# Performance work log

Hardware: AMD Instinct MI355X
Metric: run time of the kernel (lower is better)

## Reference

```python
import jax, jax.numpy as jnp
import numpy as np

N_HEADS = 4
D_K = 64

def setup_inputs() -> dict:
    key = jax.random.key(0)
    k1, k2, k3 = jax.random.split(key, 3)
    B, C, H, W = 16, 256, 32, 32
    x = jax.random.normal(k1, (B, C, H, W), dtype=jnp.float32)
    # Linear(C, 3*n_heads*d_k) stored as [in, out] for x @ W
    w_proj = jax.random.normal(k2, (C, 3 * N_HEADS * D_K), dtype=jnp.float32) * (1.0 / np.sqrt(C))
    b_proj = jnp.zeros((3 * N_HEADS * D_K,), dtype=jnp.float32)
    w_out = jax.random.normal(k3, (N_HEADS * D_K, C), dtype=jnp.float32) * (1.0 / np.sqrt(N_HEADS * D_K))
    b_out = jnp.zeros((C,), dtype=jnp.float32)
    return {"x": x, "w_proj": w_proj, "b_proj": b_proj, "w_out": w_out, "b_out": b_out}

def reference(x, w_proj, b_proj, w_out, b_out):
    B, C, H, W = x.shape
    S = H * W
    scale = D_K ** -0.5
    xs = x.reshape(B, C, S).transpose(0, 2, 1)            # [B, S, C]
    qkv = (xs @ w_proj + b_proj).reshape(B, S, N_HEADS, 3 * D_K)
    q, k, v = jnp.split(qkv, 3, axis=3)                    # each [B, S, H, dk]
    attn = jnp.einsum('bihd,bjhd->bijh', q, k) * scale     # [B, S, S, heads]
    attn = jax.nn.softmax(attn, axis=2)
    o = jnp.einsum('bijh,bjhd->bihd', attn, v)             # [B, S, heads, dk]
    o = o.reshape(B, S, N_HEADS * D_K)
    res = o @ w_out + b_out + xs                           # [B, S, C]
    return res.transpose(0, 2, 1).reshape(B, C, H, W)
```

## Files before the change

kernel.cpp:

```cpp
#include <hip/hip_runtime.h>
#include <math.h>

#define B_  16
#define C_  256
#define S_  1024
#define NH  4
#define DK  64
#define P3  768
#define ND  256

typedef unsigned short u16;
typedef unsigned int   u32;
typedef float  f32x4  __attribute__((ext_vector_type(4)));
typedef short  bf16x8 __attribute__((ext_vector_type(8)));

#define MFMA16(a, b, c) __builtin_amdgcn_mfma_f32_16x16x32_bf16(a, b, c, 0, 0, 0)

#define QSCALE 0.1803368801111137f

#define WAITVM(N) asm volatile("s_waitcnt vmcnt(" #N ")" ::: "memory")
#define BARRIER() asm volatile("s_barrier" ::: "memory")

#if __has_builtin(__builtin_amdgcn_exp2f)
#define EXP2F(x) __builtin_amdgcn_exp2f(x)
#else
#define EXP2F(x) exp2f(x)
#endif

__device__ __forceinline__ u16 f2bf(float f) {
    union { float f; u32 u; } x; x.f = f;
    u32 r = x.u + 0x7fffu + ((x.u >> 16) & 1u);
    return (u16)(r >> 16);
}

__device__ __forceinline__ u32 cvtpk(float lo, float hi) {
    u32 r;
    asm("v_cvt_pk_bf16_f32 %0, %1, %2" : "=v"(r) : "v"(lo), "v"(hi));
    return r;
}

__device__ __forceinline__ void stage16(const u16* g, u16* l) {
    __builtin_amdgcn_global_load_lds(
        (const __attribute__((address_space(1))) void*)g,
        (__attribute__((address_space(3))) void*)l, 16, 0, 0);
}

__global__ __launch_bounds__(256) void transpose_w(
    const float* __restrict__ wp, u16* __restrict__ wpT,
    const float* __restrict__ wo, u16* __restrict__ woT)
{
    const int z = blockIdx.z;
    const int Cc = z ? 256 : 768;
    if ((int)blockIdx.x * 64 >= Cc) return;
    const float* src = z ? wo : wp;
    u16* dst = z ? woT : wpT;
    const int R = 256;

    __shared__ float T[64][65];
    const int tid = threadIdx.x;
    const int c0 = blockIdx.x * 64, r0 = blockIdx.y * 64;

    const int l64 = tid & 63, rr0 = tid >> 6;
    #pragma unroll
    for (int t = 0; t < 16; ++t) {
        int rr = rr0 + t * 4;
        T[rr][l64] = src[(size_t)(r0 + rr) * Cc + c0 + l64];
    }
    __syncthreads();
    const int rp = tid & 31;
    const int cb = tid >> 5;
    #pragma unroll
    for (int t = 0; t < 8; ++t) {
        int c = cb + t * 8;
        u32 lo = f2bf(T[2 * rp][c]);
        u32 hi = f2bf(T[2 * rp + 1][c]);
        *(u32*)&dst[(size_t)(c0 + c) * R + r0 + 2 * rp] = lo | (hi << 16);
    }
}

__global__ __launch_bounds__(256, 2) void qkv_fused(
    const float* __restrict__ x, const u16* __restrict__ wpT,
    const float* __restrict__ bp, u16* __restrict__ qo,
    u16* __restrict__ ko, u16* __restrict__ vo)
{
    __shared__ __align__(16) u16 SM[40960];

    const int tid = threadIdx.x;
    const int w = tid >> 6, lane = tid & 63;
    const int n_ = lane & 15, quad = lane >> 4;

    const int id  = blockIdx.x;
    const int nid = (id & 7) * 64 + (id >> 3);
    const int hd  = nid & 3;
    const int g   = nid >> 2;
    const int s0  = (g & 7) * 128;
    const int b   = g >> 3;
    const int bh  = b * NH + hd;

    const int kq8  = tid >> 5;
    const int row4 = tid & 31;
    const float* xb = x + ((size_t)b * C_ + kq8 * 8) * S_ + s0 + row4 * 4;

    int awaddr[4];
    {
        const int kc = kq8 >> 2, quadk = kq8 & 3;
        #pragma unroll
        for (int j = 0; j < 4; ++j) {
            int row = row4 * 4 + j;
            awaddr[j] = ((row >> 4) * 2 + kc) * 512 + quadk * 128 +
                        ((((row & 15) + (row >> 4)) & 15) * 8);
        }
    }

    const u16* brp[3];
    #pragma unroll
    for (int i = 0; i < 3; ++i)
        brp[i] = wpT + (size_t)(hd * 192 + (w * 3 + i) * 16 + n_) * C_ + quad * 8;

    f32x4 acc[2][12];
    #pragma unroll
    for (int am = 0; am < 2; ++am)
        #pragma unroll
        for (int nf = 0; nf < 12; ++nf)
            #pragma unroll
            for (int r = 0; r < 4; ++r) acc[am][nf][r] = 0.f;

    float4 av[8];

    #pragma unroll
    for (int ci = 0; ci < 8; ++ci)
        av[ci] = *(const float4*)(xb + (size_t)ci * S_);
    {
        u16* Bs0 = SM + 8192;
        #pragma unroll
        for (int i = 0; i < 3; ++i) {
            stage16(brp[i],      Bs0 + ((w * 3 + i) * 2 + 0) * 512);
            stage16(brp[i] + 32, Bs0 + ((w * 3 + i) * 2 + 1) * 512);
        }
    }
    #pragma unroll
    for (int j = 0; j < 4; ++j) {
        union { bf16x8 v; u32 u[4]; } pk;
        pk.u[0] = cvtpk(av[0][j], av[1][j]);
        pk.u[1] = cvtpk(av[2][j], av[3][j]);
        pk.u[2] = cvtpk(av[4][j], av[5][j]);
        pk.u[3] = cvtpk(av[6][j], av[7][j]);
        *(bf16x8*)&SM[awaddr[j]] = pk.v;
    }
    __syncthreads();

    #pragma unroll
    for (int p = 0; p < 4; ++p) {
        u16* As_ = SM + (p & 1) * 20480;
        u16* Bs_ = As_ + 8192;
        u16* An  = SM + ((p + 1) & 1) * 20480;
        u16* Bn  = An + 8192;

        if (p < 3) {
            #pragma unroll
            for (int ci = 0; ci < 8; ++ci)
                av[ci] = *(const float4*)(xb + ((size_t)(p + 1) * 64 + ci) * S_);
            #pragma unroll
            for (int i = 0; i < 3; ++i) {
                stage16(brp[i] + (p + 1) * 64,      Bn + ((w * 3 + i) * 2 + 0) * 512);
                stage16(brp[i] + (p + 1) * 64 + 32, Bn + ((w * 3 + i) * 2 + 1) * 512);
            }
        }

        #pragma unroll
        for (int kc = 0; kc < 2; ++kc) {
            bf16x8 af0 = *(const bf16x8*)&As_[((2 * w + 0) * 2 + kc) * 512 +
                                              quad * 128 + (((n_ + 2 * w + 0) & 15) * 8)];
            bf16x8 af1 = *(const bf16x8*)&As_[((2 * w + 1) * 2 + kc) * 512 +
                                              quad * 128 + (((n_ + 2 * w + 1) & 15) * 8)];
            #pragma unroll
            for (int nf = 0; nf < 12; ++nf) {
                bf16x8 bf = *(const bf16x8*)&Bs_[(nf * 2 + kc) * 512 + lane * 8];
                acc[0][nf] = MFMA16(af0, bf, acc[0][nf]);
                acc[1][nf] = MFMA16(af1, bf, acc[1][nf]);
            }
        }

        if (p < 3) {
            #pragma unroll
            for (int j = 0; j < 4; ++j) {
                union { bf16x8 v; u32 u[4]; } pk;
                pk.u[0] = cvtpk(av[0][j], av[1][j]);
                pk.u[1] = cvtpk(av[2][j], av[3][j]);
                pk.u[2] = cvtpk(av[4][j], av[5][j]);
                pk.u[3] = cvtpk(av[6][j], av[7][j]);
                *(bf16x8*)&An[awaddr[j]] = pk.v;
            }
        }
        __syncthreads();
    }

    float bias[12];
    #pragma unroll
    for (int nf = 0; nf < 12; ++nf) bias[nf] = bp[hd * 192 + nf * 16 + n_];

    u16* Cq = SM;
    u16* Ck = SM + 9216;
    u16* Cv = SM + 18432;

    #pragma unroll
    for (int am = 0; am < 2; ++am) {
        int row0 = w * 32 + am * 16 + quad * 4;
        #pragma unroll
        for (int nf = 0; nf < 4; ++nf)
            #pragma unroll
            for (int r = 0; r < 4; ++r)
                Cq[(row0 + r) * 72 + nf * 16 + n_] =
                    f2bf((acc[am][nf][r] + bias[nf]) * QSCALE);
        #pragma unroll
        for (int nf = 4; nf < 8; ++nf)
            #pragma unroll
            for (int r = 0; r < 4; ++r)
                Ck[(row0 + r) * 72 + (nf - 4) * 16 + n_] =
                    f2bf(acc[am][nf][r] + bias[nf]);
        int colb = w * 32 + am * 16 + quad * 4;
        #pragma unroll
        for (int nf = 8; nf < 12; ++nf)
            #pragma unroll
            for (int r = 0; r < 4; ++r)
                Cv[((nf - 8) * 16 + n_) * 136 + colb + r] =
                    f2bf(acc[am][nf][r] + bias[nf]);
    }
    __syncthreads();

    #pragma unroll
    for (int t = 0; t < 4; ++t) {
        int ii = tid + t * 256;
        int row = ii >> 3, c8 = (ii & 7) * 8;
        *(bf16x8*)&qo[((size_t)bh * S_ + s0 + row) * DK + c8] =
            *(const bf16x8*)&Cq[row * 72 + c8];
        *(bf16x8*)&ko[((size_t)bh * S_ + s0 + row) * DK + c8] =
            *(const bf16x8*)&Ck[row * 72 + c8];
        int vrow = ii >> 4, vc8 = (ii & 15) * 8;
        *(bf16x8*)&vo[((size_t)bh * DK + vrow) * S_ + s0 + vc8] =
            *(const bf16x8*)&Cv[vrow * 136 + vc8];
    }
}

__global__ __launch_bounds__(256) void attn_mfma(
    const u16* __restrict__ q, const u16* __restrict__ k,
    const u16* __restrict__ vt, u16* __restrict__ obf)
{
    __shared__ __align__(16) u16 SM[32768];

    const int tid = threadIdx.x;
    const int w = tid >> 6, lane = tid & 63;
    const int n_ = lane & 15, quad = lane >> 4;

    const int id  = blockIdx.x;
    const int nid = (id & 7) * 64 + (id >> 3);
    const int i0  = (nid & 7) * 128;
    const int bh  = nid >> 3;
    const int hd  = bh & 3;
    const int b   = bh >> 2;

    bf16x8 qf[2][2];
    #pragma unroll
    for (int am = 0; am < 2; ++am) {
        const u16* qrow = q + ((size_t)bh * S_ + i0 + w * 32 + am * 16 + n_) * DK;
        qf[am][0] = *(const bf16x8*)&qrow[quad * 8];
        qf[am][1] = *(const bf16x8*)&qrow[32 + quad * 8];
    }

    union { bf16x8 v; u32 u[4]; } ones_;
    #pragma unroll
    for (int i = 0; i < 4; ++i) ones_.u[i] = 0x3F803F80u;
    const bf16x8 onesf = ones_.v;

    const int kappa = 32 * (w & 1) + 8 * (n_ >> 2) + 4 * (w >> 1) + (n_ & 3);
    const u16* kbase = k  + ((size_t)bh * S_ + kappa) * DK + quad * 8;
    const u16* vbase = vt + ((size_t)bh * DK + w * 16 + n_) * S_ + quad * 8;

    f32x4 oacc[2][4];
    f32x4 acc_sum[2];
    #pragma unroll
    for (int am = 0; am < 2; ++am) {
        #pragma unroll
        for (int nd = 0; nd < 4; ++nd)
            #pragma unroll
            for (int r = 0; r < 4; ++r) oacc[am][nd][r] = 0.f;
        #pragma unroll
        for (int r = 0; r < 4; ++r) acc_sum[am][r] = 0.f;
    }

    stage16(kbase,                SM + w * 1024);
    stage16(kbase + 32,           SM + w * 1024 + 512);
    stage16(vbase,                SM + 4096 + w * 1024);
    stage16(vbase + 32,           SM + 4096 + w * 1024 + 512);
    stage16(kbase + 64 * DK,      SM + 8192 + w * 1024);
    stage16(kbase + 64 * DK + 32, SM + 8192 + w * 1024 + 512);
    stage16(vbase + 64,           SM + 8192 + 4096 + w * 1024);
    stage16(vbase + 64 + 32,      SM + 8192 + 4096 + w * 1024 + 512);

    bf16x8 pa[2][2];

    for (int t = 0; t < 16; ++t) {
        u16* Ks = SM + (t & 3) * 8192;
        u16* Vp = SM + ((t + 3) & 3) * 8192 + 4096;
        if (t < 15) WAITVM(4); else WAITVM(0);
        BARRIER();
        if (t < 14) {
            const size_t jn = (size_t)(t + 2) * 64;
            u16* Kn = SM + ((t + 2) & 3) * 8192;
            u16* Vn = Kn + 4096;
            stage16(kbase + jn * DK,      Kn + w * 1024);
            stage16(kbase + jn * DK + 32, Kn + w * 1024 + 512);
            stage16(vbase + jn,           Vn + w * 1024);
            stage16(vbase + jn + 32,      Vn + w * 1024 + 512);
        }

        f32x4 sb[2][4];
        __builtin_amdgcn_s_setprio(1);
        #pragma unroll
        for (int nb = 0; nb < 4; ++nb) {
            bf16x8 kf0 = *(const bf16x8*)&Ks[nb * 1024 + lane * 8];
            bf16x8 kf1 = *(const bf16x8*)&Ks[nb * 1024 + 512 + lane * 8];
            #pragma unroll
            for (int am = 0; am < 2; ++am) {
                f32x4 a; a[0] = a[1] = a[2] = a[3] = 0.f;
                a = MFMA16(kf0, qf[am][0], a);
                a = MFMA16(kf1, qf[am][1], a);
                sb[am][nb] = a;
            }
        }

        if (t > 0) {
            #pragma unroll
            for (int nd = 0; nd < 4; ++nd) {
                bf16x8 vf0 = *(const bf16x8*)&Vp[nd * 1024 + lane * 8];
                bf16x8 vf1 = *(const bf16x8*)&Vp[nd * 1024 + 512 + lane * 8];
                #pragma unroll
                for (int am = 0; am < 2; ++am) {
                    oacc[am][nd] = MFMA16(vf0, pa[am][0], oacc[am][nd]);
                    oacc[am][nd] = MFMA16(vf1, pa[am][1], oacc[am][nd]);
                }
            }
            #pragma unroll
            for (int am = 0; am < 2; ++am) {
                acc_sum[am] = MFMA16(onesf, pa[am][0], acc_sum[am]);
                acc_sum[am] = MFMA16(onesf, pa[am][1], acc_sum[am]);
            }
        }
        __builtin_amdgcn_s_setprio(0);

        #pragma unroll
        for (int am = 0; am < 2; ++am) {
            float pr[4][4];
            #pragma unroll
            for (int nb = 0; nb < 4; ++nb)
                #pragma unroll
                for (int r = 0; r < 4; ++r)
                    pr[nb][r] = EXP2F(sb[am][nb][r]);
            union { bf16x8 v; u32 u[4]; } p0, p1;
            p0.u[0] = cvtpk(pr[0][0], pr[0][1]);
            p0.u[1] = cvtpk(pr[0][2], pr[0][3]);
            p0.u[2] = cvtpk(pr[2][0], pr[2][1]);
            p0.u[3] = cvtpk(pr[2][2], pr[2][3]);
            p1.u[0] = cvtpk(pr[1][0], pr[1][1]);
            p1.u[1] = cvtpk(pr[1][2], pr[1][3]);
            p1.u[2] = cvtpk(pr[3][0], pr[3][1]);
            p1.u[3] = cvtpk(pr[3][2], pr[3][3]);
            pa[am][0] = p0.v;
            pa[am][1] = p1.v;
        }
    }

    {
        u16* Vp = SM + 3 * 8192 + 4096;
        __builtin_amdgcn_s_setprio(1);
        #pragma unroll
        for (int nd = 0; nd < 4; ++nd) {
            bf16x8 vf0 = *(const bf16x8*)&Vp[nd * 1024 + lane * 8];
            bf16x8 vf1 = *(const bf16x8*)&Vp[nd * 1024 + 512 + lane * 8];
            #pragma unroll
            for (int am = 0; am < 2; ++am) {
                oacc[am][nd] = MFMA16(vf0, pa[am][0], oacc[am][nd]);
                oacc[am][nd] = MFMA16(vf1, pa[am][1], oacc[am][nd]);
            }
        }
        #pragma unroll
        for (int am = 0; am < 2; ++am) {
            acc_sum[am] = MFMA16(onesf, pa[am][0], acc_sum[am]);
            acc_sum[am] = MFMA16(onesf, pa[am][1], acc_sum[am]);
        }
        __builtin_amdgcn_s_setprio(0);
    }

    const float inv0 = 1.f / acc_sum[0][0];
    const float inv1 = 1.f / acc_sum[1][0];
    float inv[2] = {inv0, inv1};

    __syncthreads();
    u16* eb = SM + w * 2304;
    #pragma unroll
    for (int am = 0; am < 2; ++am)
        #pragma unroll
        for (int nd = 0; nd < 4; ++nd) {
            uint2 uv;
            uv.x = cvtpk(oacc[am][nd][0] * inv[am], oacc[am][nd][1] * inv[am]);
            uv.y = cvtpk(oacc[am][nd][2] * inv[am], oacc[am][nd][3] * inv[am]);
            *(uint2*)&eb[(am * 16 + n_) * 72 + nd * 16 + quad * 4] = uv;
        }
    __syncthreads();
    #pragma unroll
    for (int t = 0; t < 4; ++t) {
        int ii = lane + t * 64;
        int row = ii >> 3, c8 = (ii & 7) * 8;
        *(bf16x8*)&obf[((size_t)b * S_ + i0 + w * 32 + row) * ND + hd * DK + c8] =
            *(const bf16x8*)&eb[row * 72 + c8];
    }
}

__global__ __launch_bounds__(256) void out_proj_mfma(
    const u16* __restrict__ obf, const u16* __restrict__ woT,
    const float* __restrict__ bo, const float* __restrict__ x,
    float* __restrict__ out)
{
    __shared__ __align__(16) u16 SM[24576];

    const int tid = threadIdx.x;
    const int w = tid >> 6, lane = tid & 63;
    const int n_ = lane & 15, quad = lane >> 4;
    const int c0 = blockIdx.x * 64, s0 = blockIdx.y * 128, b = blockIdx.z;

    const u16* ar  = woT + (size_t)(c0 + w * 16 + n_) * ND + quad * 8;
    const u16* br0 = obf + ((size_t)b * S_ + s0 + (2 * w + 0) * 16 + n_) * ND + quad * 8;
    const u16* br1 = obf + ((size_t)b * S_ + s0 + (2 * w + 1) * 16 + n_) * ND + quad * 8;

    f32x4 acc[2][4];
    #pragma unroll
    for (int nf = 0; nf < 2; ++nf)
        #pragma unroll
        for (int mb = 0; mb < 4; ++mb)
            #pragma unroll
            for (int r = 0; r < 4; ++r) acc[nf][mb][r] = 0.f;

    {
        u16* Bs_ = SM;
        u16* As_ = SM + 8192;
        stage16(br0,      Bs_ + (4 * w + 0) * 512);
        stage16(br0 + 32, Bs_ + (4 * w + 1) * 512);
        stage16(br1,      Bs_ + (4 * w + 2) * 512);
        stage16(br1 + 32, Bs_ + (4 * w + 3) * 512);
        stage16(ar,       As_ + (2 * w + 0) * 512);
        stage16(ar + 32,  As_ + (2 * w + 1) * 512);
    }

    #pragma unroll
    for (int p = 0; p < 4; ++p) {
        u16* Bs_ = SM + (p & 1) * 12288;
        u16* As_ = Bs_ + 8192;
        if (p < 3) {
            const int pk = (p + 1) * 64;
            u16* Bn = SM + ((p + 1) & 1) * 12288;
            u16* An = Bn + 8192;
            stage16(br0 + pk,      Bn + (4 * w + 0) * 512);
            stage16(br0 + pk + 32, Bn + (4 * w + 1) * 512);
            stage16(br1 + pk,      Bn + (4 * w + 2) * 512);
            stage16(br1 + pk + 32, Bn + (4 * w + 3) * 512);
            stage16(ar  + pk,      An + (2 * w + 0) * 512);
            stage16(ar  + pk + 32, An + (2 * w + 1) * 512);
            WAITVM(6);
        } else {
            WAITVM(0);
        }
        BARRIER();
        #pragma unroll
        for (int kc = 0; kc < 2; ++kc) {
            bf16x8 bf0 = *(const bf16x8*)&Bs_[((2 * w + 0) * 2 + kc) * 512 + lane * 8];
            bf16x8 bf1 = *(const bf16x8*)&Bs_[((2 * w + 1) * 2 + kc) * 512 + lane * 8];
            #pragma unroll
            for (int mb = 0; mb < 4; ++mb) {
                bf16x8 af = *(const bf16x8*)&As_[(mb * 2 + kc) * 512 + lane * 8];
                acc[0][mb] = MFMA16(af, bf0, acc[0][mb]);
                acc[1][mb] = MFMA16(af, bf1, acc[1][mb]);
            }
        }
        if (p < 3) BARRIER();
    }

    #pragma unroll
    for (int mb = 0; mb < 4; ++mb)
        #pragma unroll
        for (int r = 0; r < 4; ++r) {
            int c = c0 + mb * 16 + quad * 4 + r;
            float bias = bo[c];
            #pragma unroll
            for (int nf = 0; nf < 2; ++nf) {
                size_t idx = ((size_t)b * C_ + c) * S_ + s0 + w * 32 + nf * 16 + n_;
                out[idx] = acc[nf][mb][r] + bias + x[idx];
            }
        }
}

extern "C" void kernel_launch(void* const* d_in, const int* in_sizes, int n_in,
                              void* d_out, int out_size, void* d_ws, size_t ws_size,
                              hipStream_t stream) {
    const float* x  = (const float*)d_in[0];
    const float* wp = (const float*)d_in[1];
    const float* bp = (const float*)d_in[2];
    const float* wo = (const float*)d_in[3];
    const float* bo = (const float*)d_in[4];
    float* out = (float*)d_out;

    const size_t QKV_E = (size_t)B_ * NH * S_ * DK;
    u16* q   = (u16*)d_ws;
    u16* kk  = q   + QKV_E;
    u16* vtp = kk  + QKV_E;
    u16* obf = vtp + QKV_E;
    u16* wpT = obf + (size_t)B_ * S_ * ND;
    u16* woT = wpT + (size_t)P3 * C_;

    transpose_w  <<<dim3(12, 4, 2),              256, 0, stream>>>(wp, wpT, wo, woT);
    qkv_fused    <<<dim3(512, 1, 1),             256, 0, stream>>>(x, wpT, bp, q, kk, vtp);
    attn_mfma    <<<dim3(512, 1, 1),             256, 0, stream>>>(q, kk, vtp, obf);
    out_proj_mfma<<<dim3(C_ / 64, S_ / 128, B_), 256, 0, stream>>>(obf, woT, bo, x, out);
}
```

Measured before the change: 121.6 us.

## Load K/V fragments directly into registers instead of LDS staging in attention

The attention kernel drops the four-stage LDS ring buffer for K and V and instead loads each lane's MFMA fragments straight from global memory into double-buffered registers. This removes the per-iteration barriers and the LDS round trip, and shrinks shared memory so that two blocks fit per CU (launch bounds set to 2). In exchange, latency hiding now relies on register prefetch, register pressure rises, and each wave issues redundant global loads. The out-projection kernel also gets a swizzled 1D grid mapping intended to improve L2 locality.

```diff
diff --git a/kernel.cpp b/kernel.cpp
--- a/kernel.cpp
+++ b/kernel.cpp
@@ -242,11 +242,11 @@
     }
 }
 
-__global__ __launch_bounds__(256) void attn_mfma(
+__global__ __launch_bounds__(256, 2) void attn_mfma(
     const u16* __restrict__ q, const u16* __restrict__ k,
     const u16* __restrict__ vt, u16* __restrict__ obf)
 {
-    __shared__ __align__(16) u16 SM[32768];
+    __shared__ __align__(16) u16 SM[9216];
 
     const int tid = threadIdx.x;
     const int w = tid >> 6, lane = tid & 63;
@@ -272,9 +272,9 @@
     for (int i = 0; i < 4; ++i) ones_.u[i] = 0x3F803F80u;
     const bf16x8 onesf = ones_.v;
 
-    const int kappa = 32 * (w & 1) + 8 * (n_ >> 2) + 4 * (w >> 1) + (n_ & 3);
-    const u16* kbase = k  + ((size_t)bh * S_ + kappa) * DK + quad * 8;
-    const u16* vbase = vt + ((size_t)bh * DK + w * 16 + n_) * S_ + quad * 8;
+    const int krow0 = 8 * (n_ >> 2) + (n_ & 3);
+    const u16* kb = k  + ((size_t)bh * S_ + krow0) * DK + quad * 8;
+    const u16* vb = vt + ((size_t)bh * DK + n_) * S_ + quad * 8;
 
     f32x4 oacc[2][4];
     f32x4 acc_sum[2];
@@ -288,58 +288,57 @@
         for (int r = 0; r < 4; ++r) acc_sum[am][r] = 0.f;
     }
 
-    stage16(kbase,                SM + w * 1024);
-    stage16(kbase + 32,           SM + w * 1024 + 512);
-    stage16(vbase,                SM + 4096 + w * 1024);
-    stage16(vbase + 32,           SM + 4096 + w * 1024 + 512);
-    stage16(kbase + 64 * DK,      SM + 8192 + w * 1024);
-    stage16(kbase + 64 * DK + 32, SM + 8192 + w * 1024 + 512);
-    stage16(vbase + 64,           SM + 8192 + 4096 + w * 1024);
-    stage16(vbase + 64 + 32,      SM + 8192 + 4096 + w * 1024 + 512);
-
+    bf16x8 kf[2][8], vf[2][8];
     bf16x8 pa[2][2];
 
+    #pragma unroll
+    for (int nb = 0; nb < 4; ++nb) {
+        const u16* p = kb + (size_t)(32 * (nb & 1) + 4 * (nb >> 1)) * DK;
+        kf[0][nb * 2 + 0] = *(const bf16x8*)(p);
+        kf[0][nb * 2 + 1] = *(const bf16x8*)(p + 32);
+    }
+
+    #pragma unroll 16
     for (int t = 0; t < 16; ++t) {
-        u16* Ks = SM + (t & 3) * 8192;
-        u16* Vp = SM + ((t + 3) & 3) * 8192 + 4096;
-        if (t < 15) WAITVM(4); else WAITVM(0);
-        BARRIER();
-        if (t < 14) {
-            const size_t jn = (size_t)(t + 2) * 64;
-            u16* Kn = SM + ((t + 2) & 3) * 8192;
-            u16* Vn = Kn + 4096;
-            stage16(kbase + jn * DK,      Kn + w * 1024);
-            stage16(kbase + jn * DK + 32, Kn + w * 1024 + 512);
-            stage16(vbase + jn,           Vn + w * 1024);
-            stage16(vbase + jn + 32,      Vn + w * 1024 + 512);
+        const int cur = t & 1, nxt = (t + 1) & 1;
+        if (t < 15) {
+            #pragma unroll
+            for (int nb = 0; nb < 4; ++nb) {
+                const u16* p = kb + ((size_t)(t + 1) * 64 +
+                                     32 * (nb & 1) + 4 * (nb >> 1)) * DK;
+                kf[nxt][nb * 2 + 0] = *(const bf16x8*)(p);
+                kf[nxt][nb * 2 + 1] = *(const bf16x8*)(p + 32);
+            }
+        }
+        #pragma unroll
+        for (int nd = 0; nd < 4; ++nd) {
+            const u16* p = vb + (size_t)(nd * 16) * S_ + t * 64;
+            vf[cur][nd * 2 + 0] = *(const bf16x8*)(p);
+            vf[cur][nd * 2 + 1] = *(const bf16x8*)(p + 32);
         }
 
         f32x4 sb[2][4];
         __builtin_amdgcn_s_setprio(1);
         #pragma unroll
         for (int nb = 0; nb < 4; ++nb) {
-            bf16x8 kf0 = *(const bf16x8*)&Ks[nb * 1024 + lane * 8];
-            bf16x8 kf1 = *(const bf16x8*)&Ks[nb * 1024 + 512 + lane * 8];
             #pragma unroll
             for (int am = 0; am < 2; ++am) {
                 f32x4 a; a[0] = a[1] = a[2] = a[3] = 0.f;
-                a = MFMA16(kf0, qf[am][0], a);
-                a = MFMA16(kf1, qf[am][1], a);
+                a = MFMA16(kf[cur][nb * 2 + 0], qf[am][0], a);
+                a = MFMA16(kf[cur][nb * 2 + 1], qf[am][1], a);
                 sb[am][nb] = a;
             }
         }
 
         if (t > 0) {
-            #pragma unroll
-            for (int nd = 0; nd < 4; ++nd) {
-                bf16x8 vf0 = *(const bf16x8*)&Vp[nd * 1024 + lane * 8];
-                bf16x8 vf1 = *(const bf16x8*)&Vp[nd * 1024 + 512 + lane * 8];
+            const int prv = (t - 1) & 1;
+            #pragma unroll
+            for (int nd = 0; nd < 4; ++nd)
                 #pragma unroll
                 for (int am = 0; am < 2; ++am) {
-                    oacc[am][nd] = MFMA16(vf0, pa[am][0], oacc[am][nd]);
-                    oacc[am][nd] = MFMA16(vf1, pa[am][1], oacc[am][nd]);
+                    oacc[am][nd] = MFMA16(vf[prv][nd * 2 + 0], pa[am][0], oacc[am][nd]);
+                    oacc[am][nd] = MFMA16(vf[prv][nd * 2 + 1], pa[am][1], oacc[am][nd]);
                 }
-            }
             #pragma unroll
             for (int am = 0; am < 2; ++am) {
                 acc_sum[am] = MFMA16(onesf, pa[am][0], acc_sum[am]);
@@ -371,18 +370,14 @@
     }
 
     {
-        u16* Vp = SM + 3 * 8192 + 4096;
         __builtin_amdgcn_s_setprio(1);
         #pragma unroll
-        for (int nd = 0; nd < 4; ++nd) {
-            bf16x8 vf0 = *(const bf16x8*)&Vp[nd * 1024 + lane * 8];
-            bf16x8 vf1 = *(const bf16x8*)&Vp[nd * 1024 + 512 + lane * 8];
+        for (int nd = 0; nd < 4; ++nd)
             #pragma unroll
             for (int am = 0; am < 2; ++am) {
-                oacc[am][nd] = MFMA16(vf0, pa[am][0], oacc[am][nd]);
-                oacc[am][nd] = MFMA16(vf1, pa[am][1], oacc[am][nd]);
-            }
-        }
+                oacc[am][nd] = MFMA16(vf[1][nd * 2 + 0], pa[am][0], oacc[am][nd]);
+                oacc[am][nd] = MFMA16(vf[1][nd * 2 + 1], pa[am][1], oacc[am][nd]);
+            }
         #pragma unroll
         for (int am = 0; am < 2; ++am) {
             acc_sum[am] = MFMA16(onesf, pa[am][0], acc_sum[am]);
@@ -395,7 +390,6 @@
     const float inv1 = 1.f / acc_sum[1][0];
     float inv[2] = {inv0, inv1};
 
-    __syncthreads();
     u16* eb = SM + w * 2304;
     #pragma unroll
     for (int am = 0; am < 2; ++am)
@@ -426,7 +420,13 @@
     const int tid = threadIdx.x;
     const int w = tid >> 6, lane = tid & 63;
     const int n_ = lane & 15, quad = lane >> 4;
-    const int c0 = blockIdx.x * 64, s0 = blockIdx.y * 128, b = blockIdx.z;
+
+    const int id  = blockIdx.x;
+    const int nid = (id & 7) * 64 + (id >> 3);
+    const int c0  = (nid & 3) * 64;
+    const int g   = nid >> 2;
+    const int s0  = (g & 7) * 128;
+    const int b   = g >> 3;
 
     const u16* ar  = woT + (size_t)(c0 + w * 16 + n_) * ND + quad * 8;
     const u16* br0 = obf + ((size_t)b * S_ + s0 + (2 * w + 0) * 16 + n_) * ND + quad * 8;
@@ -516,8 +516,8 @@
     u16* wpT = obf + (size_t)B_ * S_ * ND;
     u16* woT = wpT + (size_t)P3 * C_;
 
-    transpose_w  <<<dim3(12, 4, 2),              256, 0, stream>>>(wp, wpT, wo, woT);
-    qkv_fused    <<<dim3(512, 1, 1),             256, 0, stream>>>(x, wpT, bp, q, kk, vtp);
-    attn_mfma    <<<dim3(512, 1, 1),             256, 0, stream>>>(q, kk, vtp, obf);
-    out_proj_mfma<<<dim3(C_ / 64, S_ / 128, B_), 256, 0, stream>>>(obf, woT, bo, x, out);
-}
+    transpose_w  <<<dim3(12, 4, 2),  256, 0, stream>>>(wp, wpT, wo, woT);
+    qkv_fused    <<<dim3(512, 1, 1), 256, 0, stream>>>(x, wpT, bp, q, kk, vtp);
+    attn_mfma    <<<dim3(512, 1, 1), 256, 0, stream>>>(q, kk, vtp, obf);
+    out_proj_mfma<<<dim3(512, 1, 1), 256, 0, stream>>>(obf, woT, bo, x, out);
+}
```

Measured after the change: 161.5 us. 1.33x slower.
